# Performance work log

Hardware: AMD Instinct MI355X
Metric: run time of the kernel (lower is better)

The kernel has to match this reference:

```python
import jax, jax.numpy as jnp
import numpy as np

L, D, N_HEADS = 4096, 1024, 16
HEAD_D = D // N_HEADS


def setup_inputs() -> dict:
    key = jax.random.key(0)
    kx, kq, kbq, ko, kbo = jax.random.split(key, 5)
    lim_in = 1.0 / np.sqrt(D)
    return {
        "x": jax.random.normal(kx, (L, D), dtype=jnp.float32),
        # equinox nn.Linear(dim, 3*dim): weight [3D, D], bias [3D], uniform(-1/sqrt(in), 1/sqrt(in))
        "W_qkv": jax.random.uniform(kq, (3 * D, D), jnp.float32, -lim_in, lim_in),
        "b_qkv": jax.random.uniform(kbq, (3 * D,), jnp.float32, -lim_in, lim_in),
        "W_out": jax.random.uniform(ko, (D, D), jnp.float32, -lim_in, lim_in),
        "b_out": jax.random.uniform(kbo, (D,), jnp.float32, -lim_in, lim_in),
    }


def reference(x, W_qkv, b_qkv, W_out, b_out):
    # qkv projection: equinox Linear computes W @ x + b per token -> x @ W.T + b
    qkv = x @ W_qkv.T + b_qkv                         # [L, 3D]
    qkv = qkv.reshape(L, 3, N_HEADS, HEAD_D)
    qkv = jnp.transpose(qkv, (1, 2, 0, 3))            # [3, n, L, d]
    q, k, v = qkv[0], qkv[1], qkv[2]                  # each [n, L, d]

    scale = 1.0 / jnp.sqrt(jnp.asarray(HEAD_D, dtype=x.dtype))
    attn = jnp.einsum('nqd,nkd->nqk', q, k) * scale   # [n, L, L]
    causal = jnp.tril(jnp.ones((L, L), dtype=bool))
    attn = jnp.where(causal, attn, -jnp.inf)
    attn = jax.nn.softmax(attn, axis=-1)              # dropout rate 0 -> identity
    out = jnp.einsum('nqk,nkd->nqd', attn, v)         # [n, L, d]
    out = jnp.transpose(out, (1, 0, 2)).reshape(L, D)
    return out @ W_out.T + b_out                      # [L, D]
```

## Files before the change

kernel.cpp:

```cpp
#include <hip/hip_runtime.h>
#include <hip/hip_bf16.h>
#include <math.h>

#define L_SEQ 4096
#define DIM   1024
#define NH    16
#define HD    64

#define QSCL 0.18033688011112042f

typedef __attribute__((ext_vector_type(4)))  float f32x4;
typedef __attribute__((ext_vector_type(16))) float f32x16;
typedef __attribute__((ext_vector_type(8)))  short s16x8;
typedef __attribute__((ext_vector_type(4)))  short s16x4;
typedef __attribute__((ext_vector_type(4)))  unsigned u32x4;

__device__ __forceinline__ short f2bf(float f) {
  unsigned u = __builtin_bit_cast(unsigned, f);
  u = u + 0x7fffu + ((u >> 16) & 1u);
  return (short)(u >> 16);
}

__device__ __forceinline__ unsigned cvt_pk_bf16(float lo, float hi_) {
  unsigned r;
  asm("v_cvt_pk_bf16_f32 %0, %1, %2" : "=v"(r) : "v"(lo), "v"(hi_));
  return r;
}

__device__ __forceinline__ float exp2_fast(float x) {
  float r;
  asm("v_exp_f32 %0, %1" : "=v"(r) : "v"(x));
  return r;
}

__device__ __forceinline__ void gload_lds16(const void* g, void* l) {
  __builtin_amdgcn_global_load_lds(
      (__attribute__((address_space(1))) void*)(g),
      (__attribute__((address_space(3))) void*)(l), 16, 0, 0);
}

#define CVT_N1 (L_SEQ * DIM / 4)
#define CVT_N2 (3 * DIM * DIM / 4)
#define CVT_N3 (DIM * DIM / 4)

__global__ __launch_bounds__(256) void cvt_all(const float* __restrict__ x,
                                               const float* __restrict__ Wqkv,
                                               const float* __restrict__ Wout,
                                               short* __restrict__ xb,
                                               short* __restrict__ wqkvb,
                                               short* __restrict__ woutb) {
  int i = blockIdx.x * 256 + threadIdx.x;
  const float* src;
  short* dst;
  int j;
  if (i < CVT_N1)               { src = x;    dst = xb;    j = i; }
  else if (i < CVT_N1 + CVT_N2) { src = Wqkv; dst = wqkvb; j = i - CVT_N1; }
  else                          { src = Wout; dst = woutb; j = i - CVT_N1 - CVT_N2; }
  f32x4 f = *(const f32x4*)(src + j * 4);
  s16x4 o;
  o[0] = f2bf(f[0]); o[1] = f2bf(f[1]); o[2] = f2bf(f[2]); o[3] = f2bf(f[3]);
  *(s16x4*)(dst + j * 4) = o;
}


#define GEMM_MAINLOOP(A_, B_, Kdim)                                            \
  f32x4 acc[4][4];                                                             \
  _Pragma("unroll") for (int m = 0; m < 4; ++m)                                \
  _Pragma("unroll") for (int n = 0; n < 4; ++n) acc[m][n] = (f32x4)0.f;        \
  const short* aptr = A_ + (bm * 128 + w * 16 + (l >> 2)) * (Kdim) + (l & 3) * 8; \
  const short* bptr = B_ + (bn * 128 + w * 16 + (l >> 2)) * (Kdim) + (l & 3) * 8; \
  short* asl = &As[(w * 16) * 32];                                             \
  short* bsl = &Bs[(w * 16) * 32];                                             \
  for (int kk = 0; kk < (Kdim); kk += 32) {                                    \
    gload_lds16(aptr + kk, asl);                                               \
    gload_lds16(aptr + kk + 64 * (Kdim), asl + 64 * 32);                       \
    gload_lds16(bptr + kk, bsl);                                               \
    gload_lds16(bptr + kk + 64 * (Kdim), bsl + 64 * 32);                       \
    __syncthreads();                                                           \
    s16x8 af[4], bfr[4];                                                       \
    _Pragma("unroll") for (int m = 0; m < 4; ++m)                              \
      af[m] = *(const s16x8*)&As[(wr * 64 + m * 16 + lr) * 32 + lg * 8];       \
    _Pragma("unroll") for (int n = 0; n < 4; ++n)                              \
      bfr[n] = *(const s16x8*)&Bs[(wc * 64 + n * 16 + lr) * 32 + lg * 8];      \
    _Pragma("unroll") for (int m = 0; m < 4; ++m)                              \
    _Pragma("unroll") for (int n = 0; n < 4; ++n)                              \
      acc[m][n] = __builtin_amdgcn_mfma_f32_16x16x32_bf16(af[m], bfr[n], acc[m][n], 0, 0, 0); \
    __syncthreads();                                                           \
  }

__global__ __launch_bounds__(256) void gemm_qkv(const short* __restrict__ A,
                                                const short* __restrict__ B,
                                                const float* __restrict__ bias,
                                                short* __restrict__ Qb,
                                                short* __restrict__ Kf,
                                                short* __restrict__ Vf) {
  __shared__ __align__(16) short As[128 * 32];
  __shared__ __align__(16) short Bs[128 * 32];
  const int t = threadIdx.x;
  const int w = t >> 6, l = t & 63;
  const int wr = w >> 1, wc = w & 1;
  const int lr = l & 15, lg = l >> 4;
  const int bm = blockIdx.x, bn = blockIdx.y;

  GEMM_MAINLOOP(A, B, DIM)

  const int row0 = bm * 128 + wr * 64;
  const int col0 = bn * 128 + wc * 64;
#pragma unroll
  for (int n = 0; n < 4; ++n) {
    const int col = col0 + n * 16 + lr;
    const float bv = bias[col];
    const int which = col >> 10;
    const int head = (col & 1023) >> 6;
    const int d = col & 63;
    if (which == 0) {
      short* dst = Qb + (head * L_SEQ) * HD + d;
#pragma unroll
      for (int m = 0; m < 4; ++m)
#pragma unroll
        for (int j = 0; j < 4; ++j) {
          const int row = row0 + m * 16 + lg * 4 + j;
          dst[row * HD] = f2bf((acc[m][n][j] + bv) * QSCL);
        }
    } else if (which == 1) {
      const int c = d >> 4, khi = (d >> 3) & 1, e = d & 7;
      short* dst = Kf + head * (L_SEQ * HD);
#pragma unroll
      for (int m = 0; m < 4; ++m)
#pragma unroll
        for (int j = 0; j < 4; ++j) {
          const int row = row0 + m * 16 + lg * 4 + j;
          const int p = row >> 5;
          const int lane = khi * 32 + (row & 31);
          dst[((p * 4 + c) * 64 + lane) * 8 + e] = f2bf(acc[m][n][j] + bv);
        }
    } else {
      const int dh = d >> 5;
      const int dq = d & 31;
      short* dst = Vf + head * (L_SEQ * HD);
#pragma unroll
      for (int m = 0; m < 4; ++m) {
        const int rowb = row0 + m * 16 + lg * 4;
        const int tt = rowb >> 6;
        const int kc = (rowb >> 4) & 3;
        const int khi = (rowb >> 3) & 1;
        const int e0 = rowb & 7;
        s16x4 wv;
#pragma unroll
        for (int j = 0; j < 4; ++j) wv[j] = f2bf(acc[m][n][j] + bv);
        *(s16x4*)&dst[(((tt * 4 + kc) * 2 + dh) * 64 + khi * 32 + dq) * 8 + e0] = wv;
      }
    }
  }
}

__global__ __launch_bounds__(256) void gemm_out64(const short* __restrict__ A,
                                                  const short* __restrict__ B,
                                                  const float* __restrict__ bias,
                                                  float* __restrict__ C) {
  __shared__ __align__(16) short As[64 * 32];
  __shared__ __align__(16) short Bs[64 * 32];
  const int t = threadIdx.x;
  const int w = t >> 6, l = t & 63;
  const int wr = w >> 1, wc = w & 1;
  const int lr = l & 15, lg = l >> 4;
  const int bm = blockIdx.x, bn = blockIdx.y;

  f32x4 acc[2][2];
#pragma unroll
  for (int m = 0; m < 2; ++m)
#pragma unroll
    for (int n = 0; n < 2; ++n) acc[m][n] = (f32x4)0.f;

  const short* aptr = A + (bm * 64 + (t >> 2)) * DIM + (t & 3) * 8;
  const short* bptr = B + (bn * 64 + (t >> 2)) * DIM + (t & 3) * 8;
  short* asl = &As[t * 8];
  short* bsl = &Bs[t * 8];

  for (int kk = 0; kk < DIM; kk += 32) {
    gload_lds16(aptr + kk, asl);
    gload_lds16(bptr + kk, bsl);
    __syncthreads();
    s16x8 af[2], bfr[2];
#pragma unroll
    for (int m = 0; m < 2; ++m)
      af[m] = *(const s16x8*)&As[(wr * 32 + m * 16 + lr) * 32 + lg * 8];
#pragma unroll
    for (int n = 0; n < 2; ++n)
      bfr[n] = *(const s16x8*)&Bs[(wc * 32 + n * 16 + lr) * 32 + lg * 8];
#pragma unroll
    for (int m = 0; m < 2; ++m)
#pragma unroll
      for (int n = 0; n < 2; ++n)
        acc[m][n] = __builtin_amdgcn_mfma_f32_16x16x32_bf16(af[m], bfr[n], acc[m][n], 0, 0, 0);
    __syncthreads();
  }

  const int row0 = bm * 64 + wr * 32;
  const int col0 = bn * 64 + wc * 32;
#pragma unroll
  for (int n = 0; n < 2; ++n) {
    const int col = col0 + n * 16 + lr;
    const float bv = bias[col];
#pragma unroll
    for (int m = 0; m < 2; ++m)
#pragma unroll
      for (int j = 0; j < 4; ++j) {
        const int row = row0 + m * 16 + lg * 4 + j;
        C[row * DIM + col] = acc[m][n][j] + bv;
      }
  }
}

__global__ __launch_bounds__(128, 4) void attn32(const short* __restrict__ Qb,
                                                 const short* __restrict__ Kf,
                                                 const short* __restrict__ Vf,
                                                 short* __restrict__ Ob) {
  __shared__ float Mg[64 * 33];
  const int bid = blockIdx.x;
  const int xcd = bid & 7;
  const int idx = bid >> 3;
  const int head = (xcd << 1) | (idx & 1);
  const int qt = idx >> 1;
  const int qtile = (qt & 1) ? (qt >> 1) : (127 - (qt >> 1));
  const int q0 = qtile * 32;
  const int h = threadIdx.x >> 6;
  const int l = threadIdx.x & 63;
  const int q = l & 31;
  const int hi = l >> 5;

  const short* Qh = Qb + head * (L_SEQ * HD);
  const short* Kh = Kf + head * (L_SEQ * HD);
  const short* Vh = Vf + head * (L_SEQ * HD);

  s16x8 qf[4];
#pragma unroll
  for (int c = 0; c < 4; ++c)
    qf[c] = *(const s16x8*)&Qh[(q0 + q) * HD + c * 16 + hi * 8];

  f32x16 o0 = (f32x16)0.f, o1 = (f32x16)0.f;
  f32x4 lvec = (f32x4)0.f;

  const int nkt = qtile + 1;

  s16x8 kf[4];
#pragma unroll
  for (int c = 0; c < 4; ++c)
    kf[c] = *(const s16x8*)&Kh[((h * 4 + c) * 64 + l) * 8];

  for (int kt = h; kt < nkt; kt += 2) {
    s16x8 vf[2][2];
#pragma unroll
    for (int cc = 0; cc < 2; ++cc)
#pragma unroll
      for (int dh = 0; dh < 2; ++dh)
        vf[cc][dh] = *(const s16x8*)
            &Vh[((((kt >> 1) * 4 + (kt & 1) * 2 + cc) * 2 + dh) * 64 + l) * 8];

    f32x16 s = (f32x16)0.f;
#pragma unroll
    for (int c = 0; c < 4; ++c)
      s = __builtin_amdgcn_mfma_f32_32x32x16_bf16(kf[c], qf[c], s, 0, 0, 0);

    const int ktn = (kt + 2 < nkt) ? kt + 2 : kt;
#pragma unroll
    for (int c = 0; c < 4; ++c)
      kf[c] = *(const s16x8*)&Kh[((ktn * 4 + c) * 64 + l) * 8];

    if (kt == qtile) {
      const int qrel = q - hi * 4;
#pragma unroll
      for (int r = 0; r < 16; ++r) {
        const int koff = (r & 3) + 8 * (r >> 2);
        if (koff > qrel) s[r] = -1e30f;
      }
    }

#pragma unroll
    for (int r = 0; r < 16; ++r) s[r] = exp2_fast(s[r]);
#pragma unroll
    for (int r = 0; r < 16; ++r) lvec[r & 3] += s[r];

#pragma unroll
    for (int cc = 0; cc < 2; ++cc) {
      const int roff = cc * 8;
      const unsigned A = cvt_pk_bf16(s[roff + 0], s[roff + 1]);
      const unsigned B = cvt_pk_bf16(s[roff + 2], s[roff + 3]);
      const unsigned C = cvt_pk_bf16(s[roff + 4], s[roff + 5]);
      const unsigned D = cvt_pk_bf16(s[roff + 6], s[roff + 7]);
      const unsigned sA = (unsigned)__shfl_xor((int)A, 32, 64);
      const unsigned sB = (unsigned)__shfl_xor((int)B, 32, 64);
      const unsigned sC = (unsigned)__shfl_xor((int)C, 32, 64);
      const unsigned sD = (unsigned)__shfl_xor((int)D, 32, 64);
      u32x4 pw;
      pw[0] = hi ? sC : A;
      pw[1] = hi ? sD : B;
      pw[2] = hi ? C : sA;
      pw[3] = hi ? D : sB;
      const s16x8 pf = __builtin_bit_cast(s16x8, pw);
      o0 = __builtin_amdgcn_mfma_f32_32x32x16_bf16(vf[cc][0], pf, o0, 0, 0, 0);
      o1 = __builtin_amdgcn_mfma_f32_32x32x16_bf16(vf[cc][1], pf, o1, 0, 0, 0);
    }
  }

  float lsum = (lvec[0] + lvec[1]) + (lvec[2] + lvec[3]);
  lsum += __shfl_xor(lsum, 32, 64);

  if (h == 0) {
    float* st = &Mg[l * 33];
    st[0] = lsum;
#pragma unroll
    for (int r = 0; r < 16; ++r) { st[1 + r] = o0[r]; st[17 + r] = o1[r]; }
  }
  __syncthreads();
  if (h == 1) {
    const float* st = &Mg[l * 33];
    const float inv = 1.f / (st[0] + lsum);
    const int orow = q0 + q;
#pragma unroll
    for (int dh = 0; dh < 2; ++dh) {
#pragma unroll
      for (int tq = 0; tq < 4; ++tq) {
        s16x4 wv;
#pragma unroll
        for (int j = 0; j < 4; ++j) {
          const int r = tq * 4 + j;
          const float ov = (dh == 0) ? (st[1 + r] + o0[r]) : (st[17 + r] + o1[r]);
          wv[j] = f2bf(ov * inv);
        }
        *(s16x4*)&Ob[orow * DIM + head * HD + dh * 32 + tq * 8 + hi * 4] = wv;
      }
    }
  }
}

extern "C" void kernel_launch(void* const* d_in, const int* in_sizes, int n_in,
                              void* d_out, int out_size, void* d_ws, size_t ws_size,
                              hipStream_t stream) {
  const float* x    = (const float*)d_in[0];
  const float* Wqkv = (const float*)d_in[1];
  const float* bqkv = (const float*)d_in[2];
  const float* Wout = (const float*)d_in[3];
  const float* bout = (const float*)d_in[4];
  float* out = (float*)d_out;

  char* ws = (char*)d_ws;
  short* xb    = (short*)(ws);
  short* wqkvb = (short*)(ws + (8u  << 20));
  short* woutb = (short*)(ws + (14u << 20));
  short* Qb    = (short*)(ws + (16u << 20));
  short* Kf    = (short*)(ws + (24u << 20));
  short* Vf    = (short*)(ws + (32u << 20));
  short* Ob    = (short*)(ws + (40u << 20));

  cvt_all<<<(CVT_N1 + CVT_N2 + CVT_N3) / 256, 256, 0, stream>>>(x, Wqkv, Wout, xb, wqkvb, woutb);

  gemm_qkv<<<dim3(L_SEQ / 128, 3 * DIM / 128), 256, 0, stream>>>(xb, wqkvb, bqkv, Qb, Kf, Vf);
  attn32<<<2048, 128, 0, stream>>>(Qb, Kf, Vf, Ob);
  gemm_out64<<<dim3(L_SEQ / 64, DIM / 64), 256, 0, stream>>>(Ob, woutb, bout, out);
}
```

Baseline: 137.9 us.

## Split attention key loop across four waves and pair causal q-tiles per block

The attention kernel now runs four waves per block, each taking every fourth key tile instead of every second. Each block processes a complementary pair of query tiles (127-pr and pr) in sequence to balance causal work, so the grid is halved. Partial outputs from three waves are reduced through shared memory stored as packed bf16, and MFMA sections are wrapped in s_setprio. The bf16 partials lose some accuracy in the reduction, and the per-tile reduction costs an extra barrier.

Result: faster. 132.3 us (-4.0%).

```diff
diff --git a/kernel.cpp b/kernel.cpp
--- a/kernel.cpp
+++ b/kernel.cpp
@@ -212,18 +212,16 @@
   }
 }
 
-__global__ __launch_bounds__(128, 4) void attn32(const short* __restrict__ Qb,
+__global__ __launch_bounds__(256, 4) void attn32(const short* __restrict__ Qb,
                                                  const short* __restrict__ Kf,
                                                  const short* __restrict__ Vf,
                                                  short* __restrict__ Ob) {
-  __shared__ float Mg[64 * 33];
+  __shared__ unsigned Ms[3][64][17];
   const int bid = blockIdx.x;
   const int xcd = bid & 7;
   const int idx = bid >> 3;
   const int head = (xcd << 1) | (idx & 1);
-  const int qt = idx >> 1;
-  const int qtile = (qt & 1) ? (qt >> 1) : (127 - (qt >> 1));
-  const int q0 = qtile * 32;
+  const int pr = idx >> 1;
   const int h = threadIdx.x >> 6;
   const int l = threadIdx.x & 63;
   const int q = l & 31;
@@ -233,104 +231,128 @@
   const short* Kh = Kf + head * (L_SEQ * HD);
   const short* Vh = Vf + head * (L_SEQ * HD);
 
-  s16x8 qf[4];
-#pragma unroll
-  for (int c = 0; c < 4; ++c)
-    qf[c] = *(const s16x8*)&Qh[(q0 + q) * HD + c * 16 + hi * 8];
-
-  f32x16 o0 = (f32x16)0.f, o1 = (f32x16)0.f;
-  f32x4 lvec = (f32x4)0.f;
-
-  const int nkt = qtile + 1;
-
-  s16x8 kf[4];
-#pragma unroll
-  for (int c = 0; c < 4; ++c)
-    kf[c] = *(const s16x8*)&Kh[((h * 4 + c) * 64 + l) * 8];
-
-  for (int kt = h; kt < nkt; kt += 2) {
-    s16x8 vf[2][2];
-#pragma unroll
-    for (int cc = 0; cc < 2; ++cc)
-#pragma unroll
-      for (int dh = 0; dh < 2; ++dh)
-        vf[cc][dh] = *(const s16x8*)
-            &Vh[((((kt >> 1) * 4 + (kt & 1) * 2 + cc) * 2 + dh) * 64 + l) * 8];
-
-    f32x16 s = (f32x16)0.f;
+#pragma unroll 1
+  for (int ph = 0; ph < 2; ++ph) {
+    const int qtile = ph ? pr : (127 - pr);
+    const int q0 = qtile * 32;
+    const int nkt = qtile + 1;
+
+    s16x8 qf[4];
 #pragma unroll
     for (int c = 0; c < 4; ++c)
-      s = __builtin_amdgcn_mfma_f32_32x32x16_bf16(kf[c], qf[c], s, 0, 0, 0);
-
-    const int ktn = (kt + 2 < nkt) ? kt + 2 : kt;
+      qf[c] = *(const s16x8*)&Qh[(q0 + q) * HD + c * 16 + hi * 8];
+
+    f32x16 o0 = (f32x16)0.f, o1 = (f32x16)0.f;
+    f32x4 lvec = (f32x4)0.f;
+
+    s16x8 kf[4];
 #pragma unroll
     for (int c = 0; c < 4; ++c)
-      kf[c] = *(const s16x8*)&Kh[((ktn * 4 + c) * 64 + l) * 8];
-
-    if (kt == qtile) {
-      const int qrel = q - hi * 4;
-#pragma unroll
-      for (int r = 0; r < 16; ++r) {
-        const int koff = (r & 3) + 8 * (r >> 2);
-        if (koff > qrel) s[r] = -1e30f;
+      kf[c] = *(const s16x8*)&Kh[((h * 4 + c) * 64 + l) * 8];
+
+    for (int kt = h; kt < nkt; kt += 4) {
+      s16x8 vf[2][2];
+#pragma unroll
+      for (int cc = 0; cc < 2; ++cc)
+#pragma unroll
+        for (int dh = 0; dh < 2; ++dh)
+          vf[cc][dh] = *(const s16x8*)&Vh[(((kt * 2 + cc) * 2 + dh) * 64 + l) * 8];
+
+      f32x16 s = (f32x16)0.f;
+      __builtin_amdgcn_s_setprio(1);
+#pragma unroll
+      for (int c = 0; c < 4; ++c)
+        s = __builtin_amdgcn_mfma_f32_32x32x16_bf16(kf[c], qf[c], s, 0, 0, 0);
+      __builtin_amdgcn_s_setprio(0);
+
+      const int ktn = (kt + 4 < nkt) ? kt + 4 : kt;
+#pragma unroll
+      for (int c = 0; c < 4; ++c)
+        kf[c] = *(const s16x8*)&Kh[((ktn * 4 + c) * 64 + l) * 8];
+
+      if (kt == qtile) {
+        const int qrel = q - hi * 4;
+#pragma unroll
+        for (int r = 0; r < 16; ++r) {
+          const int koff = (r & 3) + 8 * (r >> 2);
+          if (koff > qrel) s[r] = -1e30f;
+        }
+      }
+
+#pragma unroll
+      for (int r = 0; r < 16; ++r) s[r] = exp2_fast(s[r]);
+#pragma unroll
+      for (int r = 0; r < 16; ++r) lvec[r & 3] += s[r];
+
+#pragma unroll
+      for (int cc = 0; cc < 2; ++cc) {
+        const int roff = cc * 8;
+        const unsigned A = cvt_pk_bf16(s[roff + 0], s[roff + 1]);
+        const unsigned B = cvt_pk_bf16(s[roff + 2], s[roff + 3]);
+        const unsigned C = cvt_pk_bf16(s[roff + 4], s[roff + 5]);
+        const unsigned D = cvt_pk_bf16(s[roff + 6], s[roff + 7]);
+        const unsigned sA = (unsigned)__shfl_xor((int)A, 32, 64);
+        const unsigned sB = (unsigned)__shfl_xor((int)B, 32, 64);
+        const unsigned sC = (unsigned)__shfl_xor((int)C, 32, 64);
+        const unsigned sD = (unsigned)__shfl_xor((int)D, 32, 64);
+        u32x4 pw;
+        pw[0] = hi ? sC : A;
+        pw[1] = hi ? sD : B;
+        pw[2] = hi ? C : sA;
+        pw[3] = hi ? D : sB;
+        const s16x8 pf = __builtin_bit_cast(s16x8, pw);
+        __builtin_amdgcn_s_setprio(1);
+        o0 = __builtin_amdgcn_mfma_f32_32x32x16_bf16(vf[cc][0], pf, o0, 0, 0, 0);
+        o1 = __builtin_amdgcn_mfma_f32_32x32x16_bf16(vf[cc][1], pf, o1, 0, 0, 0);
+        __builtin_amdgcn_s_setprio(0);
       }
     }
 
-#pragma unroll
-    for (int r = 0; r < 16; ++r) s[r] = exp2_fast(s[r]);
-#pragma unroll
-    for (int r = 0; r < 16; ++r) lvec[r & 3] += s[r];
-
-#pragma unroll
-    for (int cc = 0; cc < 2; ++cc) {
-      const int roff = cc * 8;
-      const unsigned A = cvt_pk_bf16(s[roff + 0], s[roff + 1]);
-      const unsigned B = cvt_pk_bf16(s[roff + 2], s[roff + 3]);
-      const unsigned C = cvt_pk_bf16(s[roff + 4], s[roff + 5]);
-      const unsigned D = cvt_pk_bf16(s[roff + 6], s[roff + 7]);
-      const unsigned sA = (unsigned)__shfl_xor((int)A, 32, 64);
-      const unsigned sB = (unsigned)__shfl_xor((int)B, 32, 64);
-      const unsigned sC = (unsigned)__shfl_xor((int)C, 32, 64);
-      const unsigned sD = (unsigned)__shfl_xor((int)D, 32, 64);
-      u32x4 pw;
-      pw[0] = hi ? sC : A;
-      pw[1] = hi ? sD : B;
-      pw[2] = hi ? C : sA;
-      pw[3] = hi ? D : sB;
-      const s16x8 pf = __builtin_bit_cast(s16x8, pw);
-      o0 = __builtin_amdgcn_mfma_f32_32x32x16_bf16(vf[cc][0], pf, o0, 0, 0, 0);
-      o1 = __builtin_amdgcn_mfma_f32_32x32x16_bf16(vf[cc][1], pf, o1, 0, 0, 0);
+    float lsum = (lvec[0] + lvec[1]) + (lvec[2] + lvec[3]);
+    lsum += __shfl_xor(lsum, 32, 64);
+
+    if (h > 0) {
+      unsigned* st = &Ms[h - 1][l][0];
+#pragma unroll
+      for (int w2 = 0; w2 < 8; ++w2) st[w2]     = cvt_pk_bf16(o0[2 * w2], o0[2 * w2 + 1]);
+#pragma unroll
+      for (int w2 = 0; w2 < 8; ++w2) st[8 + w2] = cvt_pk_bf16(o1[2 * w2], o1[2 * w2 + 1]);
+      st[16] = __builtin_bit_cast(unsigned, lsum);
     }
-  }
-
-  float lsum = (lvec[0] + lvec[1]) + (lvec[2] + lvec[3]);
-  lsum += __shfl_xor(lsum, 32, 64);
-
-  if (h == 0) {
-    float* st = &Mg[l * 33];
-    st[0] = lsum;
-#pragma unroll
-    for (int r = 0; r < 16; ++r) { st[1 + r] = o0[r]; st[17 + r] = o1[r]; }
-  }
-  __syncthreads();
-  if (h == 1) {
-    const float* st = &Mg[l * 33];
-    const float inv = 1.f / (st[0] + lsum);
-    const int orow = q0 + q;
-#pragma unroll
-    for (int dh = 0; dh < 2; ++dh) {
-#pragma unroll
-      for (int tq = 0; tq < 4; ++tq) {
-        s16x4 wv;
-#pragma unroll
-        for (int j = 0; j < 4; ++j) {
-          const int r = tq * 4 + j;
-          const float ov = (dh == 0) ? (st[1 + r] + o0[r]) : (st[17 + r] + o1[r]);
-          wv[j] = f2bf(ov * inv);
-        }
-        *(s16x4*)&Ob[orow * DIM + head * HD + dh * 32 + tq * 8 + hi * 4] = wv;
+    __syncthreads();
+    if (h == 0) {
+#pragma unroll
+      for (int wv = 0; wv < 3; ++wv) {
+        const unsigned* st = &Ms[wv][l][0];
+        lsum += __builtin_bit_cast(float, st[16]);
+#pragma unroll
+        for (int w2 = 0; w2 < 8; ++w2) {
+          const unsigned ua = st[w2];
+          o0[2 * w2]     += __builtin_bit_cast(float, ua << 16);
+          o0[2 * w2 + 1] += __builtin_bit_cast(float, ua & 0xffff0000u);
+          const unsigned ub = st[8 + w2];
+          o1[2 * w2]     += __builtin_bit_cast(float, ub << 16);
+          o1[2 * w2 + 1] += __builtin_bit_cast(float, ub & 0xffff0000u);
+        }
+      }
+      const float inv = 1.f / lsum;
+      const int orow = q0 + q;
+#pragma unroll
+      for (int dh = 0; dh < 2; ++dh) {
+#pragma unroll
+        for (int tq = 0; tq < 4; ++tq) {
+          s16x4 wv;
+#pragma unroll
+          for (int j = 0; j < 4; ++j) {
+            const int r = tq * 4 + j;
+            const float ov = (dh == 0) ? o0[r] : o1[r];
+            wv[j] = f2bf(ov * inv);
+          }
+          *(s16x4*)&Ob[orow * DIM + head * HD + dh * 32 + tq * 8 + hi * 4] = wv;
+        }
       }
     }
+    __syncthreads();
   }
 }
 
@@ -356,6 +378,6 @@
   cvt_all<<<(CVT_N1 + CVT_N2 + CVT_N3) / 256, 256, 0, stream>>>(x, Wqkv, Wout, xb, wqkvb, woutb);
 
   gemm_qkv<<<dim3(L_SEQ / 128, 3 * DIM / 128), 256, 0, stream>>>(xb, wqkvb, bqkv, Qb, Kf, Vf);
-  attn32<<<2048, 128, 0, stream>>>(Qb, Kf, Vf, Ob);
+  attn32<<<1024, 256, 0, stream>>>(Qb, Kf, Vf, Ob);
   gemm_out64<<<dim3(L_SEQ / 64, DIM / 64), 256, 0, stream>>>(Ob, woutb, bout, out);
 }
```
